# Kernel tuning notes

Measured on AMD Instinct MI355X. Metric: run time of the kernel, lower is better.

Reference implementation:

```python
import jax, jax.numpy as jnp
import numpy as np

DG = 4   # deformable groups
KK = 9   # 3x3 kernel
BN_EPS = 1e-5


def setup_inputs() -> dict:
    key = jax.random.key(0)
    ks = jax.random.split(key, 4)
    B, C, H, W = 4, 64, 160, 160
    fea = jax.random.normal(ks[0], (B, C, H, W), jnp.float32)
    # 1x1 offset conv (no bias) + BN (eval-mode running stats)
    w_off = jax.random.normal(ks[1], (C, C), jnp.float32) * 0.05
    bn_gamma = jnp.ones((C,), jnp.float32)
    bn_beta = jnp.zeros((C,), jnp.float32)
    bn_mean = jnp.zeros((C,), jnp.float32)
    bn_var = jnp.ones((C,), jnp.float32)
    # conv_offset_mask: 3x3 conv -> 3*DG*KK = 108 channels (o1, o2, mask)
    w_com = jax.random.normal(ks[2], (3 * DG * KK, C, 3, 3), jnp.float32) * 0.02
    b_com = jnp.zeros((3 * DG * KK,), jnp.float32)
    # modulated deformable conv main weight/bias
    w_dcn = jax.random.normal(ks[3], (C, C, 3, 3), jnp.float32) * 0.05
    b_dcn = jnp.zeros((C,), jnp.float32)
    return dict(fea=fea, w_off=w_off, bn_gamma=bn_gamma, bn_beta=bn_beta,
                bn_mean=bn_mean, bn_var=bn_var, w_com=w_com, b_com=b_com,
                w_dcn=w_dcn, b_dcn=b_dcn)


def _forward(fea, w_off, bn_gamma, bn_beta, bn_mean, bn_var, w_com, b_com, w_dcn, b_dcn):
    B, C, H, W = fea.shape
    Cg = C // DG
    # ---- offset branch: 1x1 conv + BN (eval) ----
    off_feat = jnp.einsum('bihw,oi->bohw', fea, w_off)
    inv = bn_gamma / jnp.sqrt(bn_var + BN_EPS)
    off_feat = off_feat * inv[None, :, None, None] + (bn_beta - bn_mean * inv)[None, :, None, None]
    # ---- conv_offset_mask 3x3, pad 1 ----
    com = jax.lax.conv_general_dilated(
        off_feat, w_com, (1, 1), ((1, 1), (1, 1)),
        dimension_numbers=('NCHW', 'OIHW', 'NCHW')) + b_com[None, :, None, None]
    o1, o2, m = jnp.split(com, 3, axis=1)                 # each [B, DG*KK, H, W]
    off = jnp.concatenate([o1, o2], axis=1).reshape(B, DG, KK, 2, H, W)
    dy = off[:, :, :, 0]                                  # [B, DG, KK, H, W]
    dx = off[:, :, :, 1]
    mask = jax.nn.sigmoid(m).reshape(B, DG, KK, H, W)
    # ---- sampling locations (stride=1, pad=1, dil=1) ----
    ky = (jnp.arange(KK) // 3 - 1).astype(fea.dtype)
    kx = (jnp.arange(KK) % 3 - 1).astype(fea.dtype)
    py = dy + ky[None, None, :, None, None] + jnp.arange(H, dtype=fea.dtype)[None, None, None, :, None]
    px = dx + kx[None, None, :, None, None] + jnp.arange(W, dtype=fea.dtype)[None, None, None, None, :]
    # ---- bilinear gather with zero padding outside ----
    fea_g = fea.reshape(B, DG, Cg, H * W)
    y0 = jnp.floor(py)
    x0 = jnp.floor(px)
    wy = py - y0
    wx = px - x0
    y0i = y0.astype(jnp.int32)
    x0i = x0.astype(jnp.int32)

    def corner(yi, xi, wgt):
        valid = ((yi >= 0) & (yi < H) & (xi >= 0) & (xi < W)).astype(fea.dtype)
        idx = jnp.clip(yi, 0, H - 1) * W + jnp.clip(xi, 0, W - 1)  # [B,DG,KK,H,W]
        v = jnp.take_along_axis(fea_g, idx.reshape(B, DG, 1, KK * H * W), axis=3)
        v = v.reshape(B, DG, Cg, KK, H, W)
        return v * (wgt * valid)[:, :, None]

    val = (corner(y0i,     x0i,     (1 - wy) * (1 - wx))
         + corner(y0i,     x0i + 1, (1 - wy) * wx)
         + corner(y0i + 1, x0i,     wy * (1 - wx))
         + corner(y0i + 1, x0i + 1, wy * wx))
    val = val * mask[:, :, None]                          # modulated im2col [B,DG,Cg,KK,H,W]
    # ---- deformable conv contraction + bias, relu, residual ----
    out = jnp.einsum('bgckhw,ogck->bohw', val, w_dcn.reshape(C, DG, Cg, KK)) + b_dcn[None, :, None, None]
    return fea + jax.nn.relu(out)


def reference(fea, w_off, bn_gamma, bn_beta, bn_mean, bn_var, w_com, b_com, w_dcn, b_dcn):
    return _forward(fea, w_off, bn_gamma, bn_beta, bn_mean, bn_var, w_com, b_com, w_dcn, b_dcn)
```

## Files before the change

kernel.cpp:

```cpp
#include <hip/hip_runtime.h>
#include <math.h>

#define Hc 160
#define Wc 160
#define HWc (Hc*Wc)
#define Cc 64
#define COMC 108

typedef __attribute__((ext_vector_type(8))) short short8;
typedef __attribute__((ext_vector_type(4))) float f32x4;
typedef __attribute__((ext_vector_type(2))) float f32x2;

__device__ inline short f2bf(float f) {
    union { float f; unsigned u; } v; v.f = f;
    unsigned r = (v.u + 0x7FFFu + ((v.u >> 16) & 1u)) >> 16;
    return (short)r;
}
__device__ inline float bf2f(short s) {
    union { unsigned u; float f; } v; v.u = ((unsigned)(unsigned short)s) << 16; return v.f;
}
__device__ inline float bflo(unsigned u) {
    union { unsigned u; float f; } v; v.u = u << 16; return v.f;
}
__device__ inline float bfhi(unsigned u) {
    union { unsigned u; float f; } v; v.u = u & 0xFFFF0000u; return v.f;
}
__device__ inline f32x2 bf2x2(unsigned u) {
    union { unsigned u; float f; } lo, hi;
    lo.u = u << 16; hi.u = u & 0xFFFF0000u;
    return (f32x2){lo.f, hi.f};
}
__device__ inline unsigned packbf_perm(float lo, float hi) {
    union { float f; unsigned u; } a, c; a.f = lo; c.f = hi;
    return __builtin_amdgcn_perm(c.u + 0x8000u, a.u + 0x8000u, 0x07060302u);
}

__global__ __launch_bounds__(256) void k_prep2(
    const float* __restrict__ w_off,
    const float* __restrict__ bn_g, const float* __restrict__ bn_b,
    const float* __restrict__ bn_m, const float* __restrict__ bn_v,
    const float* __restrict__ w_com, const float* __restrict__ w_dcn,
    short* __restrict__ wof_frag, float* __restrict__ shift,
    short* __restrict__ wfrag, short* __restrict__ wdT)
{
    const int t = blockIdx.x * 256 + threadIdx.x;
    if (t < 64) {
        const float scale = bn_g[t] * __frsqrt_rn(bn_v[t] + 1e-5f);
        shift[t] = bn_b[t] - bn_m[t] * scale;
    }
    if (t < 4096) {
        const int j = t & 7;
        const int lane = (t >> 3) & 63;
        const int v = t >> 9;
        const int s = v & 1, m = v >> 1;
        const int o = m*16 + (lane & 15);
        const int i = s*32 + (lane >> 4)*8 + j;
        const float scale = bn_g[o] * __frsqrt_rn(bn_v[o] + 1e-5f);
        wof_frag[t] = f2bf(w_off[o*64 + i] * scale);
    }
    if (t < 64512) {
        const int j = t & 7;
        const int lane = (t >> 3) & 63;
        const int v = t >> 9;
        const int s = v % 18, m = v / 18;
        const int kk = s >> 1, h = s & 1;
        const int o = m*16 + (lane & 15);
        const int i = h*32 + (lane >> 4)*8 + j;
        wfrag[t] = (o < COMC) ? f2bf(w_com[(o*64 + i)*9 + kk]) : (short)0;
    }
    if (t < 36864) {
        const int j = t & 7;
        const int lane = (t >> 3) & 63;
        const int v = t >> 9;
        const int s = v % 18, m = v / 18;
        const int o = m*16 + (lane & 15);
        const int q = s*32 + (lane >> 4)*8 + j;
        const int ch = q & 63, kk = q >> 6;
        wdT[t] = f2bf(w_dcn[o*576 + ch*9 + kk]);
    }
}

__global__ __launch_bounds__(256) void k_off3(
    const float* __restrict__ fea, const short* __restrict__ wof_frag,
    const float* __restrict__ shift,
    short* __restrict__ off_bf, short* __restrict__ fea_gp)
{
    __shared__ short sm[64][72];
    const int b = blockIdx.y;
    const int w = threadIdx.x >> 6, lane = threadIdx.x & 63;
    const int n = lane & 15, g = lane >> 4;
    const int p = blockIdx.x * 64 + w * 16 + n;
    const float* f = fea + (size_t)b * Cc * HWc + p;

    short8 bfrag[2];
    #pragma unroll
    for (int s = 0; s < 2; ++s) {
        #pragma unroll
        for (int j = 0; j < 8; ++j)
            bfrag[s][j] = f2bf(f[(size_t)(s*32 + g*8 + j) * HWc]);
        const int gg = s*2 + (g >> 1);
        *(short8*)&fea_gp[(((size_t)b*4 + gg)*HWc + p)*16 + (g & 1)*8] = bfrag[s];
    }

    f32x4 acc[4];
    #pragma unroll
    for (int m = 0; m < 4; ++m) acc[m] = (f32x4){0.f, 0.f, 0.f, 0.f};
    #pragma unroll
    for (int s = 0; s < 2; ++s) {
        #pragma unroll
        for (int m = 0; m < 4; ++m) {
            const short8 afrag = *(const short8*)&wof_frag[((m*2 + s)*64 + lane)*8];
            acc[m] = __builtin_amdgcn_mfma_f32_16x16x32_bf16(afrag, bfrag[s], acc[m], 0, 0, 0);
        }
    }
    #pragma unroll
    for (int m = 0; m < 4; ++m) {
        #pragma unroll
        for (int r = 0; r < 4; ++r) {
            const int o = m*16 + g*4 + r;
            sm[w*16 + n][o] = f2bf(acc[m][r] + shift[o]);
        }
    }
    __syncthreads();
    for (int q = threadIdx.x; q < 512; q += 256) {
        const int pl = q >> 3, sc = q & 7;
        *(uint4*)&off_bf[((size_t)(b * HWc) + blockIdx.x*64 + pl)*64 + sc*8] =
            *(const uint4*)&sm[pl][sc*8];
    }
}

#define SWZ(px, sc) ((sc) ^ ((px) & 7))

__global__ __launch_bounds__(256) void k_com6(
    const short* __restrict__ off_bf, const short* __restrict__ wfrag,
    const float* __restrict__ b_com, short* __restrict__ com_rec)
{
    __shared__ short smem[14336];
    const int seg = blockIdx.x;
    const int yb  = blockIdx.y * 4;
    const int b   = blockIdx.z;
    const int x0  = seg * 32;
    const int tid = threadIdx.x;

    for (int c = tid; c < 1632; c += 256) {
        const int r   = c / 272;
        const int rem = c - r * 272;
        const int px  = rem >> 3;
        const int sc  = rem & 7;
        const int gy  = yb + r - 1;
        const int gx  = x0 + px - 1;
        uint4 vv = make_uint4(0u, 0u, 0u, 0u);
        if ((unsigned)gy < (unsigned)Hc && (unsigned)gx < (unsigned)Wc)
            vv = *(const uint4*)&off_bf[(((size_t)b * HWc + gy * Wc + gx) << 6) + (sc << 3)];
        *(uint4*)&smem[((r*34 + px)*8 + SWZ(px, sc)) * 8] = vv;
    }
    __syncthreads();

    const int w    = tid >> 6;
    const int lane = tid & 63;
    const int n15  = lane & 15;
    const int g    = lane >> 4;
    const int m0   = w * 2;
    const int nm   = (w == 3) ? 1 : 2;

    f32x4 acc[2][8];
    #pragma unroll
    for (int mm = 0; mm < 2; ++mm)
        #pragma unroll
        for (int t = 0; t < 8; ++t) acc[mm][t] = (f32x4){0.f, 0.f, 0.f, 0.f};

    #pragma unroll
    for (int kk = 0; kk < 9; ++kk) {
        #pragma unroll
        for (int h = 0; h < 2; ++h) {
            const int s = kk*2 + h;
            const int slot = h*4 + g;
            short8 bf[8];
            #pragma unroll
            for (int t = 0; t < 8; ++t) {
                const int r  = t >> 1, xt = t & 1;
                const int ry = r + kk/3;
                const int rx = xt*16 + n15 + (kk % 3);
                bf[t] = *(const short8*)&smem[((ry*34 + rx)*8 + SWZ(rx, slot)) * 8];
            }
            #pragma unroll
            for (int mm = 0; mm < 2; ++mm) {
                if (mm < nm) {
                    const short8 afrag =
                        *(const short8*)&wfrag[(((m0+mm)*18 + s)*64 + lane)*8];
                    #pragma unroll
                    for (int t = 0; t < 8; ++t)
                        acc[mm][t] = __builtin_amdgcn_mfma_f32_16x16x32_bf16(
                            afrag, bf[t], acc[mm][t], 0, 0, 0);
                }
            }
        }
    }
    __syncthreads();

    #pragma unroll
    for (int mm = 0; mm < 2; ++mm) {
        if (mm < nm) {
            #pragma unroll
            for (int r4 = 0; r4 < 4; ++r4) {
                const int oc = (m0+mm)*16 + g*4 + r4;
                if (oc < COMC) {
                    int pos;
                    if (oc < 72) pos = oc;
                    else { const int q = oc - 72; pos = 72 + (q/9)*10 + (q - (q/9)*9); }
                    const float bo = b_com[oc];
                    #pragma unroll
                    for (int t = 0; t < 8; ++t) {
                        const int r = t >> 1, xt = t & 1;
                        smem[(r*32 + xt*16 + n15)*112 + pos] = f2bf(acc[mm][t][r4] + bo);
                    }
                }
            }
        }
    }
    __syncthreads();

    for (int c = tid; c < 1792; c += 256) {
        const int pr = c / 14, ch = c - pr * 14;
        const int r = pr >> 5, pxl = pr & 31;
        const int p = (yb + r) * Wc + x0 + pxl;
        *(uint4*)&com_rec[((size_t)b * HWc + p)*112 + ch*8] = *(const uint4*)&smem[pr*112 + ch*8];
    }
}

#define SROW 360
#define SG   (7*SROW)

__global__ __launch_bounds__(256, 4) void k_dcn11(
    const float* __restrict__ fea, const short* __restrict__ com_rec,
    const short* __restrict__ fea_gp, const short* __restrict__ wdT,
    const float* __restrict__ b_dcn, float* __restrict__ out)
{
    __shared__ short stage_s[4*SG];
    __shared__ short val_s[9216];
    const int nx = gridDim.x;
    int bid = blockIdx.x;
    bid = (bid & 7) * (nx >> 3) + (bid >> 3);
    const int b = blockIdx.y;
    const int base = bid * 16;
    const int ty = base / Wc;
    const int tx = base - ty * Wc;
    const int tid = threadIdx.x;
    const int w = tid >> 6, lane = tid & 63;
    const int n = lane & 15, g2 = lane >> 4;

    const size_t outb = ((size_t)b * Cc + (w*16 + g2*4)) * HWc + base + n;
    float resv[4], biasv[4];
    #pragma unroll
    for (int r = 0; r < 4; ++r) {
        resv[r]  = fea[outb + (size_t)r * HWc];
        biasv[r] = b_dcn[w*16 + g2*4 + r];
    }

    const int ns = (w < 2) ? 3 : (w == 2 ? 2 : 1);
    const int sbase = (w <= 2) ? w * 192 : 512;
    int sk[3];
    const int sg = (lane >> 4) & 3;
    const int sl = lane & 15;
    unsigned sdydx[3]; float smk[3];
    #pragma unroll
    for (int i = 0; i < 3; ++i) {
        sk[i] = (sbase + i*64 + lane) >> 6;
        if (i < ns) {
            const short* crp = &com_rec[((size_t)b * HWc + base + sl) * 112];
            sdydx[i] = *(const unsigned*)&crp[sg*18 + 2*sk[i]];
            smk[i]   = bf2f(crp[72 + sg*10 + sk[i]]);
        }
    }

    if (lane < 44) {
        const int c = lane >> 1, h = lane & 1;
        const int gx = min(max(tx - 3 + c, 0), Wc-1);
        const short* src = fea_gp + (((size_t)b*4 + w)*HWc)*16;
        #pragma unroll
        for (int r = 0; r < 7; ++r) {
            const int gy = min(max(ty - 3 + r, 0), Hc-1);
            *(uint4*)&stage_s[w*SG + r*SROW + c*16 + h*8] =
                *(const uint4*)&src[(gy*Wc + gx)*16 + h*8];
        }
    }
    __syncthreads();

    #pragma unroll
    for (int i = 0; i < 3; ++i) {
        if (i < ns) {
            const int k = sk[i];
            const float dy = bflo(sdydx[i]), dx = bfhi(sdydx[i]);
            const float mk = 1.f / (1.f + __expf(-smk[i]));
            const float py  = dy + (float)(k/3 - 1 + ty);
            const float pxf = dx + (float)(k%3 - 1 + tx + sl);
            const float y0f = floorf(py), x0f = floorf(pxf);
            const float wy = py - y0f, wx = pxf - x0f;
            const int y0 = (int)y0f, x0i = (int)x0f;
            const int y1 = y0 + 1,  x1 = x0i + 1;
            const bool vy0 = (y0 >= 0) & (y0 < Hc);
            const bool vy1 = (y1 >= 0) & (y1 < Hc);
            const bool vx0 = (x0i >= 0) & (x0i < Wc);
            const bool vx1 = (x1 >= 0) & (x1 < Wc);
            const float c00 = (vy0 && vx0) ? (1.f-wy)*(1.f-wx)*mk : 0.f;
            const float c01 = (vy0 && vx1) ? (1.f-wy)*wx*mk       : 0.f;
            const float c10 = (vy1 && vx0) ? wy*(1.f-wx)*mk       : 0.f;
            const float c11 = (vy1 && vx1) ? wy*wx*mk             : 0.f;
            const int y0c = min(max(y0, 0), Hc-1), y1c = min(max(y1, 0), Hc-1);
            const int x0c = min(max(x0i, 0), Wc-1), x1c = min(max(x1, 0), Wc-1);
            const int wr0 = min(max(y0c - (ty-3), 0), 6);
            const int wr1 = min(max(y1c - (ty-3), 0), 6);
            const int wc0 = min(max(x0c - (tx-3), 0), 21);
            const int wc1 = min(max(x1c - (tx-3), 0), 21);
            const short* sgp = &stage_s[sg*SG];
            const short* r00 = sgp + wr0*SROW + wc0*16;
            const short* r01 = sgp + wr0*SROW + wc1*16;
            const short* r10 = sgp + wr1*SROW + wc0*16;
            const short* r11 = sgp + wr1*SROW + wc1*16;
            const uint4 a00 = *(const uint4*)r00, b00 = *(const uint4*)(r00 + 8);
            const uint4 a01 = *(const uint4*)r01, b01 = *(const uint4*)(r01 + 8);
            const uint4 a10 = *(const uint4*)r10, b10 = *(const uint4*)(r10 + 8);
            const uint4 a11 = *(const uint4*)r11, b11 = *(const uint4*)(r11 + 8);
            unsigned uo[8];
            {
                const unsigned* p00 = (const unsigned*)&a00;
                const unsigned* p01 = (const unsigned*)&a01;
                const unsigned* p10 = (const unsigned*)&a10;
                const unsigned* p11 = (const unsigned*)&a11;
                #pragma unroll
                for (int wi = 0; wi < 4; ++wi) {
                    const f32x2 v = bf2x2(p00[wi])*c00 + bf2x2(p01[wi])*c01
                                  + bf2x2(p10[wi])*c10 + bf2x2(p11[wi])*c11;
                    uo[wi] = packbf_perm(v.x, v.y);
                }
            }
            {
                const unsigned* p00 = (const unsigned*)&b00;
                const unsigned* p01 = (const unsigned*)&b01;
                const unsigned* p10 = (const unsigned*)&b10;
                const unsigned* p11 = (const unsigned*)&b11;
                #pragma unroll
                for (int wi = 0; wi < 4; ++wi) {
                    const f32x2 v = bf2x2(p00[wi])*c00 + bf2x2(p01[wi])*c01
                                  + bf2x2(p10[wi])*c10 + bf2x2(p11[wi])*c11;
                    uo[4 + wi] = packbf_perm(v.x, v.y);
                }
            }
            const int cc = k*8 + sg*2;
            *(uint4*)&val_s[((cc    )*16 + sl) * 8] = make_uint4(uo[0], uo[1], uo[2], uo[3]);
            *(uint4*)&val_s[((cc + 1)*16 + sl) * 8] = make_uint4(uo[4], uo[5], uo[6], uo[7]);
        }
    }
    __syncthreads();

    f32x4 acc = (f32x4){0.f, 0.f, 0.f, 0.f};
    const short* wp = wdT + ((w*18)*64 + lane)*8;
    __builtin_amdgcn_s_setprio(1);
    #pragma unroll
    for (int s = 0; s < 18; ++s) {
        const short8 bfrag = *(const short8*)&val_s[((s*4 + g2)*16 + n) * 8];
        const short8 afrag = *(const short8*)&wp[(s*64) * 8];
        acc = __builtin_amdgcn_mfma_f32_16x16x32_bf16(afrag, bfrag, acc, 0, 0, 0);
    }
    __builtin_amdgcn_s_setprio(0);
    #pragma unroll
    for (int r = 0; r < 4; ++r)
        out[outb + (size_t)r * HWc] = resv[r] + fmaxf(acc[r] + biasv[r], 0.f);
}

extern "C" void kernel_launch(void* const* d_in, const int* in_sizes, int n_in,
                              void* d_out, int out_size, void* d_ws, size_t ws_size,
                              hipStream_t stream) {
    const float* fea   = (const float*)d_in[0];
    const float* w_off = (const float*)d_in[1];
    const float* bn_g  = (const float*)d_in[2];
    const float* bn_b  = (const float*)d_in[3];
    const float* bn_m  = (const float*)d_in[4];
    const float* bn_v  = (const float*)d_in[5];
    const float* w_com = (const float*)d_in[6];
    const float* b_com = (const float*)d_in[7];
    const float* w_dcn = (const float*)d_in[8];
    const float* b_dcn = (const float*)d_in[9];
    float* out = (float*)d_out;

    char* ws = (char*)d_ws;
    short* com_rec  = (short*)ws;
    short* off_bf   = (short*)(ws + 22937600);
    short* fea_gp   = (short*)(ws + 36044800);
    short* wfrag    = (short*)(ws + 49152000);
    short* wdT      = (short*)(ws + 49281024);
    short* wof_frag = (short*)(ws + 49354752);
    float* shift    = (float*)(ws + 49362944);

    k_prep2<<<252, 256, 0, stream>>>(w_off, bn_g, bn_b, bn_m, bn_v,
                                     w_com, w_dcn, wof_frag, shift, wfrag, wdT);

    dim3 gA(HWc / 64, 4);
    k_off3<<<gA, 256, 0, stream>>>(fea, wof_frag, shift, off_bf, fea_gp);

    dim3 gB(5, Hc / 4, 4);
    k_com6<<<gB, 256, 0, stream>>>(off_bf, wfrag, b_com, com_rec);

    dim3 gC(HWc / 16, 4);
    k_dcn11<<<gC, 256, 0, stream>>>(fea, com_rec, fea_gp, wdT, b_dcn, out);
}
```

Before: 97.77 us.

## Fold 1x1 offset conv and BN into 3x3 conv weights with border bias correction

```diff
diff --git a/kernel.cpp b/kernel.cpp
--- a/kernel.cpp
+++ b/kernel.cpp
@@ -35,29 +35,34 @@
     return __builtin_amdgcn_perm(c.u + 0x8000u, a.u + 0x8000u, 0x07060302u);
 }
 
-__global__ __launch_bounds__(256) void k_prep2(
-    const float* __restrict__ w_off,
+__global__ __launch_bounds__(256) void k_prep_a(
+    const float* __restrict__ w_off, const float* __restrict__ bn_g,
+    const float* __restrict__ bn_v, const float* __restrict__ w_com,
+    float* __restrict__ Wtmp)
+{
+    const int t = blockIdx.x * 256 + threadIdx.x;
+    if (t >= 108*64*9) return;
+    const int o = t / 576;
+    const int rem = t - o * 576;
+    const int c = rem / 9;
+    const int kk = rem - c * 9;
+    float acc = 0.f;
+    for (int i = 0; i < 64; ++i) {
+        const float scale = bn_g[i] * __frsqrt_rn(bn_v[i] + 1e-5f);
+        acc += w_com[(o*64 + i)*9 + kk] * scale * w_off[i*64 + c];
+    }
+    Wtmp[t] = acc;
+}
+
+__global__ __launch_bounds__(256) void k_prep_b(
     const float* __restrict__ bn_g, const float* __restrict__ bn_b,
     const float* __restrict__ bn_m, const float* __restrict__ bn_v,
     const float* __restrict__ w_com, const float* __restrict__ w_dcn,
-    short* __restrict__ wof_frag, float* __restrict__ shift,
-    short* __restrict__ wfrag, short* __restrict__ wdT)
+    const float* __restrict__ b_com, const float* __restrict__ Wtmp,
+    short* __restrict__ wfrag, short* __restrict__ wdT,
+    float* __restrict__ bfull, float* __restrict__ S9)
 {
     const int t = blockIdx.x * 256 + threadIdx.x;
-    if (t < 64) {
-        const float scale = bn_g[t] * __frsqrt_rn(bn_v[t] + 1e-5f);
-        shift[t] = bn_b[t] - bn_m[t] * scale;
-    }
-    if (t < 4096) {
-        const int j = t & 7;
-        const int lane = (t >> 3) & 63;
-        const int v = t >> 9;
-        const int s = v & 1, m = v >> 1;
-        const int o = m*16 + (lane & 15);
-        const int i = s*32 + (lane >> 4)*8 + j;
-        const float scale = bn_g[o] * __frsqrt_rn(bn_v[o] + 1e-5f);
-        wof_frag[t] = f2bf(w_off[o*64 + i] * scale);
-    }
     if (t < 64512) {
         const int j = t & 7;
         const int lane = (t >> 3) & 63;
@@ -65,8 +70,8 @@
         const int s = v % 18, m = v / 18;
         const int kk = s >> 1, h = s & 1;
         const int o = m*16 + (lane & 15);
-        const int i = h*32 + (lane >> 4)*8 + j;
-        wfrag[t] = (o < COMC) ? f2bf(w_com[(o*64 + i)*9 + kk]) : (short)0;
+        const int c = h*32 + (lane >> 4)*8 + j;
+        wfrag[t] = (o < COMC) ? f2bf(Wtmp[(o*64 + c)*9 + kk]) : (short)0;
     }
     if (t < 36864) {
         const int j = t & 7;
@@ -78,62 +83,48 @@
         const int ch = q & 63, kk = q >> 6;
         wdT[t] = f2bf(w_dcn[o*576 + ch*9 + kk]);
     }
-}
-
-__global__ __launch_bounds__(256) void k_off3(
-    const float* __restrict__ fea, const short* __restrict__ wof_frag,
-    const float* __restrict__ shift,
-    short* __restrict__ off_bf, short* __restrict__ fea_gp)
+    if (t < COMC) {
+        float S[9];
+        #pragma unroll
+        for (int k = 0; k < 9; ++k) S[k] = 0.f;
+        for (int i = 0; i < 64; ++i) {
+            const float scale = bn_g[i] * __frsqrt_rn(bn_v[i] + 1e-5f);
+            const float sh = bn_b[i] - bn_m[i] * scale;
+            #pragma unroll
+            for (int k = 0; k < 9; ++k) S[k] += w_com[(t*64 + i)*9 + k] * sh;
+        }
+        float full = b_com[t];
+        #pragma unroll
+        for (int k = 0; k < 9; ++k) { full += S[k]; S9[t*9 + k] = S[k]; }
+        bfull[t] = full;
+    }
+}
+
+__global__ __launch_bounds__(256) void k_repack(
+    const float* __restrict__ fea, short* __restrict__ fea_gp)
 {
-    __shared__ short sm[64][72];
     const int b = blockIdx.y;
-    const int w = threadIdx.x >> 6, lane = threadIdx.x & 63;
-    const int n = lane & 15, g = lane >> 4;
-    const int p = blockIdx.x * 64 + w * 16 + n;
+    const int p = blockIdx.x * 256 + threadIdx.x;
     const float* f = fea + (size_t)b * Cc * HWc + p;
-
-    short8 bfrag[2];
-    #pragma unroll
-    for (int s = 0; s < 2; ++s) {
+    #pragma unroll
+    for (int g = 0; g < 4; ++g) {
+        unsigned uo[8];
         #pragma unroll
         for (int j = 0; j < 8; ++j)
-            bfrag[s][j] = f2bf(f[(size_t)(s*32 + g*8 + j) * HWc]);
-        const int gg = s*2 + (g >> 1);
-        *(short8*)&fea_gp[(((size_t)b*4 + gg)*HWc + p)*16 + (g & 1)*8] = bfrag[s];
-    }
-
-    f32x4 acc[4];
-    #pragma unroll
-    for (int m = 0; m < 4; ++m) acc[m] = (f32x4){0.f, 0.f, 0.f, 0.f};
-    #pragma unroll
-    for (int s = 0; s < 2; ++s) {
-        #pragma unroll
-        for (int m = 0; m < 4; ++m) {
-            const short8 afrag = *(const short8*)&wof_frag[((m*2 + s)*64 + lane)*8];
-            acc[m] = __builtin_amdgcn_mfma_f32_16x16x32_bf16(afrag, bfrag[s], acc[m], 0, 0, 0);
-        }
-    }
-    #pragma unroll
-    for (int m = 0; m < 4; ++m) {
-        #pragma unroll
-        for (int r = 0; r < 4; ++r) {
-            const int o = m*16 + g*4 + r;
-            sm[w*16 + n][o] = f2bf(acc[m][r] + shift[o]);
-        }
-    }
-    __syncthreads();
-    for (int q = threadIdx.x; q < 512; q += 256) {
-        const int pl = q >> 3, sc = q & 7;
-        *(uint4*)&off_bf[((size_t)(b * HWc) + blockIdx.x*64 + pl)*64 + sc*8] =
-            *(const uint4*)&sm[pl][sc*8];
+            uo[j] = packbf_perm(f[(size_t)(g*16 + 2*j) * HWc],
+                                f[(size_t)(g*16 + 2*j + 1) * HWc]);
+        short* dst = fea_gp + (((size_t)b*4 + g)*HWc + p)*16;
+        *(uint4*)dst       = make_uint4(uo[0], uo[1], uo[2], uo[3]);
+        *(uint4*)(dst + 8) = make_uint4(uo[4], uo[5], uo[6], uo[7]);
     }
 }
 
 #define SWZ(px, sc) ((sc) ^ ((px) & 7))
 
-__global__ __launch_bounds__(256) void k_com6(
-    const short* __restrict__ off_bf, const short* __restrict__ wfrag,
-    const float* __restrict__ b_com, short* __restrict__ com_rec)
+__global__ __launch_bounds__(256) void k_com8(
+    const short* __restrict__ fea_gp, const short* __restrict__ wfrag,
+    const float* __restrict__ bfull, const float* __restrict__ S9,
+    short* __restrict__ com_rec)
 {
     __shared__ short smem[14336];
     const int seg = blockIdx.x;
@@ -151,7 +142,7 @@
         const int gx  = x0 + px - 1;
         uint4 vv = make_uint4(0u, 0u, 0u, 0u);
         if ((unsigned)gy < (unsigned)Hc && (unsigned)gx < (unsigned)Wc)
-            vv = *(const uint4*)&off_bf[(((size_t)b * HWc + gy * Wc + gx) << 6) + (sc << 3)];
+            vv = *(const uint4*)&fea_gp[(((size_t)b*4 + (sc >> 1))*HWc + gy*Wc + gx)*16 + (sc & 1)*8];
         *(uint4*)&smem[((r*34 + px)*8 + SWZ(px, sc)) * 8] = vv;
     }
     __syncthreads();
@@ -198,6 +189,10 @@
     }
     __syncthreads();
 
+    const bool btop = (yb == 0), bbot = (yb == Hc-4);
+    const bool bleft = (seg == 0), bright = (seg == 4);
+    const bool interior = !(btop | bbot | bleft | bright);
+
     #pragma unroll
     for (int mm = 0; mm < 2; ++mm) {
         if (mm < nm) {
@@ -208,11 +203,34 @@
                     int pos;
                     if (oc < 72) pos = oc;
                     else { const int q = oc - 72; pos = 72 + (q/9)*10 + (q - (q/9)*9); }
-                    const float bo = b_com[oc];
-                    #pragma unroll
-                    for (int t = 0; t < 8; ++t) {
-                        const int r = t >> 1, xt = t & 1;
-                        smem[(r*32 + xt*16 + n15)*112 + pos] = f2bf(acc[mm][t][r4] + bo);
+                    const float bias0 = bfull[oc];
+                    if (interior) {
+                        #pragma unroll
+                        for (int t = 0; t < 8; ++t) {
+                            const int r = t >> 1, xt = t & 1;
+                            smem[(r*32 + xt*16 + n15)*112 + pos] = f2bf(acc[mm][t][r4] + bias0);
+                        }
+                    } else {
+                        const float* s9 = &S9[oc*9];
+                        #pragma unroll
+                        for (int t = 0; t < 8; ++t) {
+                            const int r = t >> 1, xt = t & 1;
+                            const int y = yb + r, x = x0 + xt*16 + n15;
+                            float bb = bias0;
+                            if (y == 0)    bb -= s9[0] + s9[1] + s9[2];
+                            if (y == Hc-1) bb -= s9[6] + s9[7] + s9[8];
+                            if (x == 0) {
+                                bb -= s9[0] + s9[3] + s9[6];
+                                if (y == 0) bb += s9[0];
+                                if (y == Hc-1) bb += s9[6];
+                            }
+                            if (x == Wc-1) {
+                                bb -= s9[2] + s9[5] + s9[8];
+                                if (y == 0) bb += s9[2];
+                                if (y == Hc-1) bb += s9[8];
+                            }
+                            smem[(r*32 + xt*16 + n15)*112 + pos] = f2bf(acc[mm][t][r4] + bb);
+                        }
                     }
                 }
             }
@@ -384,22 +402,23 @@
     float* out = (float*)d_out;
 
     char* ws = (char*)d_ws;
-    short* com_rec  = (short*)ws;
-    short* off_bf   = (short*)(ws + 22937600);
-    short* fea_gp   = (short*)(ws + 36044800);
-    short* wfrag    = (short*)(ws + 49152000);
-    short* wdT      = (short*)(ws + 49281024);
-    short* wof_frag = (short*)(ws + 49354752);
-    float* shift    = (float*)(ws + 49362944);
-
-    k_prep2<<<252, 256, 0, stream>>>(w_off, bn_g, bn_b, bn_m, bn_v,
-                                     w_com, w_dcn, wof_frag, shift, wfrag, wdT);
-
-    dim3 gA(HWc / 64, 4);
-    k_off3<<<gA, 256, 0, stream>>>(fea, wof_frag, shift, off_bf, fea_gp);
+    short* com_rec = (short*)ws;
+    short* fea_gp  = (short*)(ws + 22937600);
+    short* wfrag   = (short*)(ws + 36044800);
+    short* wdT     = (short*)(ws + 36173824);
+    float* Wtmp    = (float*)(ws + 36247552);
+    float* bfull   = (float*)(ws + 36496384);
+    float* S9      = (float*)(ws + 36496816);
+
+    k_prep_a<<<243, 256, 0, stream>>>(w_off, bn_g, bn_v, w_com, Wtmp);
+    k_prep_b<<<252, 256, 0, stream>>>(bn_g, bn_b, bn_m, bn_v, w_com, w_dcn,
+                                      b_com, Wtmp, wfrag, wdT, bfull, S9);
+
+    dim3 gR(HWc / 256, 4);
+    k_repack<<<gR, 256, 0, stream>>>(fea, fea_gp);
 
     dim3 gB(5, Hc / 4, 4);
-    k_com6<<<gB, 256, 0, stream>>>(off_bf, wfrag, b_com, com_rec);
+    k_com8<<<gB, 256, 0, stream>>>(fea_gp, wfrag, bfull, S9, com_rec);
 
     dim3 gC(HWc / 16, 4);
     k_dcn11<<<gC, 256, 0, stream>>>(fea, com_rec, fea_gp, wdT, b_dcn, out);
```

New measurement: 118.5 us. 21.3% more time.
